# Kernel tuning notes

Measured on AMD Instinct MI355X. Metric: run time of the kernel, lower is better.

## Reference

```python
import jax, jax.numpy as jnp
import numpy as np

B, C, H, W = 4, 256, 64, 64
IC = C // 2  # inter_channels default = in_channels // 2


def setup_inputs() -> dict:
    key = jax.random.key(0)
    ks = jax.random.split(key, 7)
    x = jax.random.normal(ks[0], (B, C, H, W), dtype=jnp.float32)
    s = 0.02
    Wq = jax.random.normal(ks[1], (IC, C), dtype=jnp.float32) * s
    bq = jnp.zeros((IC,), dtype=jnp.float32)
    Wk = jax.random.normal(ks[2], (IC, C), dtype=jnp.float32) * s
    bk = jnp.zeros((IC,), dtype=jnp.float32)
    Wv = jax.random.normal(ks[3], (C, C), dtype=jnp.float32) * s
    bv = jnp.zeros((C,), dtype=jnp.float32)
    gamma = jnp.full((1,), 0.1, dtype=jnp.float32)  # nn.Parameter; init 0 in torch, 0.1 here for nontrivial grads
    return {"x": x, "Wq": Wq, "bq": bq, "Wk": Wk, "bk": bk, "Wv": Wv, "bv": bv, "gamma": gamma}


def reference(x, Wq, bq, Wk, bk, Wv, bv, gamma):
    b, c, h, w = x.shape
    n = h * w
    # 1x1 conv projections == per-pixel linear layers
    q = jnp.einsum('bchw,oc->bohw', x, Wq) + bq[None, :, None, None]  # [B,IC,H,W]
    k = jnp.einsum('bchw,oc->bohw', x, Wk) + bk[None, :, None, None]
    v = jnp.einsum('bchw,oc->bohw', x, Wv) + bv[None, :, None, None]  # [B,C,H,W]
    q = q.reshape(b, IC, n).transpose(0, 2, 1)  # [B,N,IC]
    k = k.reshape(b, IC, n)                     # [B,IC,N]
    v = v.reshape(b, c, n)                      # [B,C,N]
    scale = jnp.asarray(IC, x.dtype) ** -0.5
    energy = jnp.einsum('bni,bim->bnm', q, k) * scale  # [B,N,N]
    attn = jax.nn.softmax(energy, axis=-1)             # dropout is identity in eval
    # torch: out = bmm(value, attention.transpose(-1,-2)) -> out[b,c,i] = sum_j v[b,c,j]*attn[b,i,j]
    out = jnp.einsum('bcj,bij->bci', v, attn).reshape(b, c, h, w)
    return gamma[0] * out + 2.0 * x
```

## Files before the change

kernel.cpp:

```cpp
#include <hip/hip_runtime.h>
#include <stdint.h>


#define Bn 4
#define Cn 256
#define ICn 128
#define Nn 4096

typedef __attribute__((ext_vector_type(8))) short bf16x8;
typedef __attribute__((ext_vector_type(4))) float f32x4;
typedef __attribute__((ext_vector_type(16))) float f32x16;

__device__ __forceinline__ unsigned short f2bf(float f) {
  union { float f; uint32_t u; } v; v.f = f;
  uint32_t r = (v.u + 0x7fffu + ((v.u >> 16) & 1u)) >> 16;
  return (unsigned short)r;
}

__device__ __forceinline__ uint32_t pk4_fp8(float a, float b, float c, float d) {
  int r = 0;
  r = __builtin_amdgcn_cvt_pk_fp8_f32(a, b, r, false);
  r = __builtin_amdgcn_cvt_pk_fp8_f32(c, d, r, true);
  return (uint32_t)r;
}

__global__ __launch_bounds__(256) void cvt_weights(const float* __restrict__ Wq,
                                                   const float* __restrict__ Wk,
                                                   const float* __restrict__ Wv,
                                                   unsigned short* __restrict__ wbf) {
  int t = blockIdx.x * 256 + threadIdx.x;
  int tile = t >> 9;
  int kk = (t >> 6) & 7;
  int lane = t & 63;
  const float* W; int row;
  if (tile < 8)       { W = Wq; row = tile * 16 + (lane & 15); }
  else if (tile < 16) { W = Wk; row = (tile - 8) * 16 + (lane & 15); }
  else                { W = Wv; row = (tile - 16) * 16 + (lane & 15); }
  const float* src = W + (size_t)row * Cn + kk * 32 + (lane >> 4) * 8;
  float4 f0 = *(const float4*)src;
  float4 f1 = *(const float4*)(src + 4);
  ushort4 o0, o1;
  o0.x = f2bf(f0.x); o0.y = f2bf(f0.y); o0.z = f2bf(f0.z); o0.w = f2bf(f0.w);
  o1.x = f2bf(f1.x); o1.y = f2bf(f1.y); o1.z = f2bf(f1.z); o1.w = f2bf(f1.w);
  *(ushort4*)(wbf + (size_t)t * 8)     = o0;
  *(ushort4*)(wbf + (size_t)t * 8 + 4) = o1;
}

__global__ __launch_bounds__(256, 2) void proj_kernel(const float* __restrict__ x,
                                                      const unsigned short* __restrict__ wbf,
                                                      const float* __restrict__ bq,
                                                      const float* __restrict__ bk,
                                                      const float* __restrict__ bv,
                                                      uint8_t* __restrict__ qF,
                                                      uint8_t* __restrict__ kF,
                                                      uint8_t* __restrict__ vF) {
  const int b = blockIdx.y;
  const int ntile = blockIdx.x;
  const int px0 = ntile * 32;
  const int tid = threadIdx.x;
  const int lane = tid & 63;
  const int w = tid >> 6;
  const int c0 = lane & 15, g = lane >> 4;
  const float hscale = 0.3570958292f;

  __shared__ __align__(16) unsigned short xT[32][264];

  #pragma unroll
  for (int t = 0; t < 8; ++t) {
    int c = (tid >> 3) + t * 32;
    int i8 = tid & 7;
    float4 f4 = *(const float4*)(x + ((size_t)(b * Cn + c)) * Nn + px0 + i8 * 4);
    xT[i8 * 4 + 0][c] = f2bf(f4.x);
    xT[i8 * 4 + 1][c] = f2bf(f4.y);
    xT[i8 * 4 + 2][c] = f2bf(f4.z);
    xT[i8 * 4 + 3][c] = f2bf(f4.w);
  }
  __syncthreads();

  bf16x8 a[2][8];
  #pragma unroll
  for (int h = 0; h < 2; ++h)
    #pragma unroll
    for (int kk = 0; kk < 8; ++kk)
      a[h][kk] = *(const bf16x8*)&xT[h * 16 + c0][kk * 32 + g * 8];

  f32x4 zero = {0.f, 0.f, 0.f, 0.f};

  if (w < 2) {
    const int isq = (w == 0);
    const float* bias = isq ? bq : bk;
    uint8_t* dst = isq ? qF : kF;
    #pragma unroll
    for (int otl = 0; otl < 8; ++otl) {
      const int wt = (isq ? 0 : 8) + otl;
      bf16x8 wf[8];
      #pragma unroll
      for (int kk = 0; kk < 8; ++kk)
        wf[kk] = *(const bf16x8*)(wbf + (((size_t)wt * 8 + kk) << 9) + lane * 8);
      float4 bz = *(const float4*)(bias + otl * 16 + g * 4);
      #pragma unroll
      for (int h = 0; h < 2; ++h) {
        f32x4 acc = zero;
        #pragma unroll
        for (int kk = 0; kk < 8; ++kk)
          acc = __builtin_amdgcn_mfma_f32_16x16x32_bf16(wf[kk], a[h][kk], acc, 0, 0, 0);
        uint32_t d = pk4_fp8((acc[0] + bz.x) * hscale, (acc[1] + bz.y) * hscale,
                             (acc[2] + bz.z) * hscale, (acc[3] + bz.w) * hscale);
        size_t idx = (((((size_t)b * 128 + ntile) * 4 + (otl >> 1)) * 2 + (g >> 1)) * 32
                      + (h * 16 + c0)) * 16 + (otl & 1) * 8 + (g & 1) * 4;
        *(uint32_t*)(dst + idx) = d;
      }
    }
  } else {
    #pragma unroll
    for (int oi = 0; oi < 8; ++oi) {
      const int vtg = (w - 2) * 8 + oi;
      bf16x8 wf[8];
      #pragma unroll
      for (int kk = 0; kk < 8; ++kk)
        wf[kk] = *(const bf16x8*)(wbf + (((size_t)(16 + vtg) * 8 + kk) << 9) + lane * 8);
      const float bias = bv[vtg * 16 + c0];
      #pragma unroll
      for (int h = 0; h < 2; ++h) {
        f32x4 acc = zero;
        #pragma unroll
        for (int kk = 0; kk < 8; ++kk)
          acc = __builtin_amdgcn_mfma_f32_16x16x32_bf16(a[h][kk], wf[kk], acc, 0, 0, 0);
        uint32_t d = pk4_fp8(acc[0] + bias, acc[1] + bias, acc[2] + bias, acc[3] + bias);
        size_t idx = ((((size_t)b * 128 + ntile) * 8 + (vtg >> 1)) * 64
                      + (g >> 1) * 32 + (vtg & 1) * 16 + c0) * 16 + h * 8 + (g & 1) * 4;
        *(uint32_t*)(vF + idx) = d;
      }
    }
  }
}

__global__ __launch_bounds__(256, 2) void attn_kernel(const uint8_t* __restrict__ qF,
                                                      const uint8_t* __restrict__ kF,
                                                      const uint8_t* __restrict__ vF,
                                                      const float* __restrict__ x,
                                                      const float* __restrict__ gamma,
                                                      float* __restrict__ out) {
  const int blk = blockIdx.x;
  const int b = (blk & 7) >> 1;
  const int rg = (blk >> 3) | ((blk & 1) << 6);
  const int n0 = rg * 32;
  const int tid = threadIdx.x;
  const int L = tid & 63;
  const int ks = tid >> 6;
  const int l31 = L & 31, l5 = L >> 5;
  const bool lo = (l5 == 0);

  __shared__ __align__(16) struct SM {
    float obuf[256][33];
    float lsum[4][32];
  } sm;

  long qf[8];
  {
    const uint8_t* qp = qF + ((size_t)(b * 128 + rg) << 12) + L * 16;
    #pragma unroll
    for (int t = 0; t < 4; ++t) {
      union { uint4 u4; struct { uint64_t lo, hi; } s; } u;
      u.u4 = *(const uint4*)(qp + t * 1024);
      qf[2 * t] = (long)u.s.lo; qf[2 * t + 1] = (long)u.s.hi;
    }
  }

  f32x16 oacc[8];
  #pragma unroll
  for (int ct = 0; ct < 8; ++ct)
    #pragma unroll
    for (int i = 0; i < 16; ++i) oacc[ct][i] = 0.f;
  float lacc = 0.f;

  const uint8_t* kBase = kF + (((size_t)b * 128) << 12) + L * 16;
  const uint8_t* vBase = vF + (((size_t)b * 128) << 13) + L * 16;

  long kfr[8];
  {
    const uint8_t* kp = kBase + (((size_t)(ks * 32)) << 12);
    #pragma unroll
    for (int t = 0; t < 4; ++t) {
      union { uint4 u4; struct { uint64_t lo, hi; } s; } u;
      u.u4 = *(const uint4*)(kp + t * 1024);
      kfr[2 * t] = (long)u.s.lo; kfr[2 * t + 1] = (long)u.s.hi;
    }
  }

  for (int it = 0; it < 32; ++it) {
    const int kb = ks * 32 + it;

    uint4 vfr[8];
    {
      const uint8_t* vp = vBase + ((size_t)kb << 13);
      #pragma unroll
      for (int ct = 0; ct < 8; ++ct) vfr[ct] = *(const uint4*)(vp + ct * 1024);
    }

    f32x16 s;
    #pragma unroll
    for (int i = 0; i < 16; ++i) s[i] = 0.f;
    #pragma unroll
    for (int f = 0; f < 8; ++f)
      s = __builtin_amdgcn_mfma_f32_32x32x16_fp8_fp8(kfr[f], qf[f], s, 0, 0, 0);

    if (it < 31) {
      const uint8_t* kp = kBase + (((size_t)(kb + 1)) << 12);
      #pragma unroll
      for (int t = 0; t < 4; ++t) {
        union { uint4 u4; struct { uint64_t lo, hi; } s; } u;
        u.u4 = *(const uint4*)(kp + t * 1024);
        kfr[2 * t] = (long)u.s.lo; kfr[2 * t + 1] = (long)u.s.hi;
      }
    }

    #pragma unroll
    for (int i = 0; i < 16; ++i) {
      float r;
      asm("v_exp_f32 %0, %1" : "=v"(r) : "v"(s[i]));
      s[i] = r;
    }
    #pragma unroll
    for (int i = 0; i < 16; ++i) lacc += s[i];
    uint32_t d0 = pk4_fp8(s[0], s[1], s[2], s[3]);
    uint32_t d1 = pk4_fp8(s[4], s[5], s[6], s[7]);
    uint32_t d2 = pk4_fp8(s[8], s[9], s[10], s[11]);
    uint32_t d3 = pk4_fp8(s[12], s[13], s[14], s[15]);

    uint32_t a0 = d1, b0 = d0;
    asm("v_permlane32_swap_b32 %0, %1" : "+v"(a0), "+v"(b0));
    long f0 = (long)(((uint64_t)a0 << 32) | b0);
    uint32_t a1 = d3, b1 = d2;
    asm("v_permlane32_swap_b32 %0, %1" : "+v"(a1), "+v"(b1));
    long f1 = (long)(((uint64_t)a1 << 32) | b1);

    #pragma unroll
    for (int ct = 0; ct < 8; ++ct) {
      union { uint4 u4; struct { uint64_t lo, hi; } s; } u;
      u.u4 = vfr[ct];
      oacc[ct] = __builtin_amdgcn_mfma_f32_32x32x16_fp8_fp8((long)u.s.lo, f0, oacc[ct], 0, 0, 0);
      oacc[ct] = __builtin_amdgcn_mfma_f32_32x32x16_fp8_fp8((long)u.s.hi, f1, oacc[ct], 0, 0, 0);
    }
  }

  float lfin = lacc + __shfl_xor(lacc, 32, 64);

  #pragma unroll
  for (int pq = 0; pq < 4; ++pq) {
    __syncthreads();
    if (pq == 0 && lo) sm.lsum[ks][l31] = lfin;
    if (ks == pq) {
      #pragma unroll
      for (int ct = 0; ct < 8; ++ct) {
        #pragma unroll
        for (int i = 0; i < 16; ++i) {
          int ch = ct * 32 + (i & 3) + 8 * (i >> 2) + 4 * l5;
          if (pq == 0) sm.obuf[ch][l31] = oacc[ct][i];
          else         sm.obuf[ch][l31] += oacc[ct][i];
        }
      }
    }
  }
  __syncthreads();

  const int row = tid & 31;
  const float coef = gamma[0] / (sm.lsum[0][row] + sm.lsum[1][row] +
                                 sm.lsum[2][row] + sm.lsum[3][row]);
  #pragma unroll 4
  for (int t = 0; t < 32; ++t) {
    int ch = (tid >> 5) + t * 8;
    size_t off = ((size_t)(b * Cn + ch)) * Nn + n0 + row;
    out[off] = sm.obuf[ch][row] * coef + 2.0f * x[off];
  }
}

extern "C" void kernel_launch(void* const* d_in, const int* in_sizes, int n_in,
                              void* d_out, int out_size, void* d_ws, size_t ws_size,
                              hipStream_t stream) {
  const float* x     = (const float*)d_in[0];
  const float* Wq    = (const float*)d_in[1];
  const float* bq    = (const float*)d_in[2];
  const float* Wk    = (const float*)d_in[3];
  const float* bk    = (const float*)d_in[4];
  const float* Wv    = (const float*)d_in[5];
  const float* bv    = (const float*)d_in[6];
  const float* gamma = (const float*)d_in[7];
  float* out = (float*)d_out;

  uint8_t* qF = (uint8_t*)d_ws;
  uint8_t* kF = qF + (2u << 20);
  uint8_t* vF = kF + (2u << 20);
  unsigned short* wbf = (unsigned short*)(vF + (4u << 20));

  hipLaunchKernelGGL(cvt_weights, dim3(64), dim3(256), 0, stream, Wq, Wk, Wv, wbf);
  hipLaunchKernelGGL(proj_kernel, dim3(128, 4), dim3(256), 0, stream,
                     x, wbf, bq, bk, bv, qF, kF, vF);
  hipLaunchKernelGGL(attn_kernel, dim3(512), dim3(256), 0, stream,
                     qF, kF, vF, x, gamma, out);
}
```

Before: 136.8 us.

## Switch attention MFMAs to scaled 32x32x64 FP8 and relayout Q/K/V fragments

Replaces the 32x32x16 FP8 MFMAs with the MI355X block-scaled 32x32x64 f8f6f4 MFMA using unit scales, for both QK^T and PV. Each iteration now processes 64 keys as two 32-key score tiles whose packed probabilities are permlane-swapped into one 64-wide K operand. The projection kernel's Q/K/V fp8 output layouts are rewritten to match the new operand fragment shapes, and the loop count halves. The explicit K prefetch of the next iteration is dropped, which could expose load latency. Register pressure also rises with vA/vB and kv arrays.

```diff
diff --git a/kernel.cpp b/kernel.cpp
--- a/kernel.cpp
+++ b/kernel.cpp
@@ -10,6 +10,9 @@
 typedef __attribute__((ext_vector_type(8))) short bf16x8;
 typedef __attribute__((ext_vector_type(4))) float f32x4;
 typedef __attribute__((ext_vector_type(16))) float f32x16;
+typedef __attribute__((ext_vector_type(8))) int i32x8;
+
+#define SCALE1 0x7f7f7f7f
 
 __device__ __forceinline__ unsigned short f2bf(float f) {
   union { float f; uint32_t u; } v; v.f = f;
@@ -106,8 +109,9 @@
           acc = __builtin_amdgcn_mfma_f32_16x16x32_bf16(wf[kk], a[h][kk], acc, 0, 0, 0);
         uint32_t d = pk4_fp8((acc[0] + bz.x) * hscale, (acc[1] + bz.y) * hscale,
                              (acc[2] + bz.z) * hscale, (acc[3] + bz.w) * hscale);
-        size_t idx = (((((size_t)b * 128 + ntile) * 4 + (otl >> 1)) * 2 + (g >> 1)) * 32
-                      + (h * 16 + c0)) * 16 + (otl & 1) * 8 + (g & 1) * 4;
+        int D = otl * 4 + g;
+        size_t idx = (((size_t)(b * 128 + ntile) * 2 + (D >> 4)) << 11)
+                   + (size_t)(((((D >> 3) & 1) * 32) + h * 16 + c0) * 32 + (D & 7) * 4);
         *(uint32_t*)(dst + idx) = d;
       }
     }
@@ -127,8 +131,9 @@
         for (int kk = 0; kk < 8; ++kk)
           acc = __builtin_amdgcn_mfma_f32_16x16x32_bf16(a[h][kk], wf[kk], acc, 0, 0, 0);
         uint32_t d = pk4_fp8(acc[0] + bias, acc[1] + bias, acc[2] + bias, acc[3] + bias);
-        size_t idx = ((((size_t)b * 128 + ntile) * 8 + (vtg >> 1)) * 64
-                      + (g >> 1) * 32 + (vtg & 1) * 16 + c0) * 16 + h * 8 + (g & 1) * 4;
+        int pos = (ntile & 1) * 32 + h * 16 + g * 4;
+        size_t idx = (((size_t)(b * 64 + (ntile >> 1)) * 8 + (vtg >> 1)) << 11)
+                   + (size_t)(((pos >> 5) * 32 + (vtg & 1) * 16 + c0) * 32 + ((pos >> 2) & 7) * 4);
         *(uint32_t*)(vF + idx) = d;
       }
     }
@@ -156,14 +161,15 @@
     float lsum[4][32];
   } sm;
 
-  long qf[8];
+  i32x8 qv[2];
   {
-    const uint8_t* qp = qF + ((size_t)(b * 128 + rg) << 12) + L * 16;
-    #pragma unroll
-    for (int t = 0; t < 4; ++t) {
-      union { uint4 u4; struct { uint64_t lo, hi; } s; } u;
-      u.u4 = *(const uint4*)(qp + t * 1024);
-      qf[2 * t] = (long)u.s.lo; qf[2 * t + 1] = (long)u.s.hi;
+    const uint8_t* qp = qF + ((size_t)(b * 128 + rg) * 2) * 2048 + L * 32;
+    #pragma unroll
+    for (int mf = 0; mf < 2; ++mf) {
+      union { uint4 u[2]; i32x8 v; } u;
+      u.u[0] = *(const uint4*)(qp + mf * 2048);
+      u.u[1] = *(const uint4*)(qp + mf * 2048 + 16);
+      qv[mf] = u.v;
     }
   }
 
@@ -174,47 +180,34 @@
     for (int i = 0; i < 16; ++i) oacc[ct][i] = 0.f;
   float lacc = 0.f;
 
-  const uint8_t* kBase = kF + (((size_t)b * 128) << 12) + L * 16;
-  const uint8_t* vBase = vF + (((size_t)b * 128) << 13) + L * 16;
-
-  long kfr[8];
-  {
-    const uint8_t* kp = kBase + (((size_t)(ks * 32)) << 12);
-    #pragma unroll
-    for (int t = 0; t < 4; ++t) {
-      union { uint4 u4; struct { uint64_t lo, hi; } s; } u;
-      u.u4 = *(const uint4*)(kp + t * 1024);
-      kfr[2 * t] = (long)u.s.lo; kfr[2 * t + 1] = (long)u.s.hi;
-    }
-  }
-
-  for (int it = 0; it < 32; ++it) {
-    const int kb = ks * 32 + it;
-
-    uint4 vfr[8];
+  const uint8_t* kBase = kF + ((size_t)(b * 128) * 2) * 2048 + L * 32;
+  const uint8_t* vBase = vF + ((size_t)(b * 64) * 8) * 2048 + L * 32;
+
+  for (int it = 0; it < 16; ++it) {
+    const int kb = ks * 16 + it;
+
+    i32x8 kv[4];
     {
-      const uint8_t* vp = vBase + ((size_t)kb << 13);
-      #pragma unroll
-      for (int ct = 0; ct < 8; ++ct) vfr[ct] = *(const uint4*)(vp + ct * 1024);
-    }
+      const uint8_t* kp = kBase + (size_t)kb * 8192;
+      #pragma unroll
+      for (int f = 0; f < 4; ++f) {
+        union { uint4 u[2]; i32x8 v; } u;
+        u.u[0] = *(const uint4*)(kp + f * 2048);
+        u.u[1] = *(const uint4*)(kp + f * 2048 + 16);
+        kv[f] = u.v;
+      }
+    }
+
+    const uint8_t* vp = vBase + (size_t)kb * 16384;
+    uint4 vA[8], vB[8];
+    #pragma unroll
+    for (int ct = 0; ct < 8; ++ct) vA[ct] = *(const uint4*)(vp + ct * 2048);
 
     f32x16 s;
     #pragma unroll
     for (int i = 0; i < 16; ++i) s[i] = 0.f;
-    #pragma unroll
-    for (int f = 0; f < 8; ++f)
-      s = __builtin_amdgcn_mfma_f32_32x32x16_fp8_fp8(kfr[f], qf[f], s, 0, 0, 0);
-
-    if (it < 31) {
-      const uint8_t* kp = kBase + (((size_t)(kb + 1)) << 12);
-      #pragma unroll
-      for (int t = 0; t < 4; ++t) {
-        union { uint4 u4; struct { uint64_t lo, hi; } s; } u;
-        u.u4 = *(const uint4*)(kp + t * 1024);
-        kfr[2 * t] = (long)u.s.lo; kfr[2 * t + 1] = (long)u.s.hi;
-      }
-    }
-
+    s = __builtin_amdgcn_mfma_scale_f32_32x32x64_f8f6f4(kv[0], qv[0], s, 0, 0, 0, SCALE1, 0, SCALE1);
+    s = __builtin_amdgcn_mfma_scale_f32_32x32x64_f8f6f4(kv[1], qv[1], s, 0, 0, 0, SCALE1, 0, SCALE1);
     #pragma unroll
     for (int i = 0; i < 16; ++i) {
       float r;
@@ -228,19 +221,48 @@
     uint32_t d2 = pk4_fp8(s[8], s[9], s[10], s[11]);
     uint32_t d3 = pk4_fp8(s[12], s[13], s[14], s[15]);
 
-    uint32_t a0 = d1, b0 = d0;
-    asm("v_permlane32_swap_b32 %0, %1" : "+v"(a0), "+v"(b0));
-    long f0 = (long)(((uint64_t)a0 << 32) | b0);
-    uint32_t a1 = d3, b1 = d2;
-    asm("v_permlane32_swap_b32 %0, %1" : "+v"(a1), "+v"(b1));
-    long f1 = (long)(((uint64_t)a1 << 32) | b1);
+    #pragma unroll
+    for (int i = 0; i < 16; ++i) s[i] = 0.f;
+    s = __builtin_amdgcn_mfma_scale_f32_32x32x64_f8f6f4(kv[2], qv[0], s, 0, 0, 0, SCALE1, 0, SCALE1);
+    s = __builtin_amdgcn_mfma_scale_f32_32x32x64_f8f6f4(kv[3], qv[1], s, 0, 0, 0, SCALE1, 0, SCALE1);
+
+    #pragma unroll
+    for (int ct = 0; ct < 8; ++ct) vB[ct] = *(const uint4*)(vp + ct * 2048 + 16);
+
+    #pragma unroll
+    for (int i = 0; i < 16; ++i) {
+      float r;
+      asm("v_exp_f32 %0, %1" : "=v"(r) : "v"(s[i]));
+      s[i] = r;
+    }
+    #pragma unroll
+    for (int i = 0; i < 16; ++i) lacc += s[i];
+    uint32_t e0 = pk4_fp8(s[0], s[1], s[2], s[3]);
+    uint32_t e1 = pk4_fp8(s[4], s[5], s[6], s[7]);
+    uint32_t e2 = pk4_fp8(s[8], s[9], s[10], s[11]);
+    uint32_t e3 = pk4_fp8(s[12], s[13], s[14], s[15]);
+
+    union { uint32_t w[8]; i32x8 v; } pf;
+    {
+      uint32_t a0 = e0, b0 = d0;
+      asm("v_permlane32_swap_b32 %0, %1" : "+v"(a0), "+v"(b0));
+      pf.w[0] = b0; pf.w[1] = a0;
+      uint32_t a1 = e1, b1 = d1;
+      asm("v_permlane32_swap_b32 %0, %1" : "+v"(a1), "+v"(b1));
+      pf.w[2] = b1; pf.w[3] = a1;
+      uint32_t a2 = e2, b2 = d2;
+      asm("v_permlane32_swap_b32 %0, %1" : "+v"(a2), "+v"(b2));
+      pf.w[4] = b2; pf.w[5] = a2;
+      uint32_t a3 = e3, b3 = d3;
+      asm("v_permlane32_swap_b32 %0, %1" : "+v"(a3), "+v"(b3));
+      pf.w[6] = b3; pf.w[7] = a3;
+    }
 
     #pragma unroll
     for (int ct = 0; ct < 8; ++ct) {
-      union { uint4 u4; struct { uint64_t lo, hi; } s; } u;
-      u.u4 = vfr[ct];
-      oacc[ct] = __builtin_amdgcn_mfma_f32_32x32x16_fp8_fp8((long)u.s.lo, f0, oacc[ct], 0, 0, 0);
-      oacc[ct] = __builtin_amdgcn_mfma_f32_32x32x16_fp8_fp8((long)u.s.hi, f1, oacc[ct], 0, 0, 0);
+      union { uint4 u[2]; i32x8 v; } va;
+      va.u[0] = vA[ct]; va.u[1] = vB[ct];
+      oacc[ct] = __builtin_amdgcn_mfma_scale_f32_32x32x64_f8f6f4(va.v, pf.v, oacc[ct], 0, 0, 0, SCALE1, 0, SCALE1);
     }
   }
 
```

Result: faster. 133.9 us (-2.1%).
